# Optimization experiments

Hardware: AMD Instinct MI355X
Metric: run time of the kernel (lower is better)

## Reference

```python
import jax, jax.numpy as jnp
import numpy as np

NUM_HEADS = 32
HEAD_DIM = 128
NUM_KV_HEADS = 8
SCALE = 0.08838834764831845  # 1/sqrt(128)
SEQ_LEN = 2048
TOTAL_TOKENS = 4096  # batch=2 sequences of 2048


def setup_inputs() -> dict:
    key = jax.random.key(0)
    kq, kk, kv = jax.random.split(key, 3)
    q = jax.random.normal(kq, (TOTAL_TOKENS, NUM_HEADS * HEAD_DIM), dtype=jnp.float32)
    k = jax.random.normal(kk, (TOTAL_TOKENS, NUM_KV_HEADS * HEAD_DIM), dtype=jnp.float32)
    v = jax.random.normal(kv, (TOTAL_TOKENS, NUM_KV_HEADS * HEAD_DIM), dtype=jnp.float32)
    return {"q": q, "k": k, "v": v, "seq_len": SEQ_LEN}


def reference(q, k, v, seq_len):
    # Unified (varlen) causal GQA attention: flattened tokens are split into
    # batch sequences of equal length (the prefill path of the unified kernel).
    T = q.shape[0]
    B = T // seq_len
    G = NUM_HEADS // NUM_KV_HEADS  # query heads per kv head
    # [B, S, Hkv, G, D] and [B, S, Hkv, D]
    qh = q.reshape(B, seq_len, NUM_KV_HEADS, G, HEAD_DIM)
    kh = k.reshape(B, seq_len, NUM_KV_HEADS, HEAD_DIM)
    vh = v.reshape(B, seq_len, NUM_KV_HEADS, HEAD_DIM)
    # scores: [B, Hkv, G, Sq, Sk]
    scores = jnp.einsum("bqhgd,bkhd->bhgqk", qh, kh) * SCALE
    causal = jnp.tril(jnp.ones((seq_len, seq_len), dtype=bool))
    scores = jnp.where(causal, scores, jnp.finfo(scores.dtype).min)
    probs = jax.nn.softmax(scores, axis=-1)
    # out: [B, Sq, Hkv, G, D]
    o = jnp.einsum("bhgqk,bkhd->bqhgd", probs, vh)
    return o.reshape(T, NUM_HEADS * HEAD_DIM)
```

## Files before the change

kernel.cpp:

```cpp
#include <hip/hip_runtime.h>
#include <stdint.h>
#include <stddef.h>


#define S_LEN   2048
#define HQ      32
#define HKV     8
#define DH      128
#define QSTRIDE (HQ*DH)
#define KSTRIDE (HKV*DH)
#define SCALE_L2 0.12751139830213113f

#define KTILE      64
#define NTILES     (S_LEN/KTILE)
#define CSTRIDE    520
#define KPART      (16*CSTRIDE)
#define TILE_ELEMS (KPART + 16*CSTRIDE)

typedef __bf16 bf16;
typedef short        s16x4 __attribute__((ext_vector_type(4)));
typedef short        s16x8 __attribute__((ext_vector_type(8)));
typedef float        f32x4 __attribute__((ext_vector_type(4)));
typedef unsigned int u32x4 __attribute__((ext_vector_type(4)));

__device__ __forceinline__ unsigned int pk2(float a, float b) {
  union { bf16 h[2]; unsigned int u; } x;
  x.h[0] = (bf16)a; x.h[1] = (bf16)b;
  return x.u;
}

__device__ __forceinline__ int koff(int chunk, int key) {
  return chunk*CSTRIDE + key*8;
}
__device__ __forceinline__ int voff(int unit, int d) {
  return KPART + unit*CSTRIDE + d*4;
}

__global__ __launch_bounds__(512, 4)
void attn_fwd(const float* __restrict__ qg, const float* __restrict__ kg,
              const float* __restrict__ vg, float* __restrict__ og) {
  __shared__ bf16 smem[2*TILE_ELEMS];

  const int tid   = threadIdx.x;
  const int lane  = tid & 63;
  const int wave  = tid >> 6;
  const int l15   = lane & 15;
  const int quad  = lane >> 4;
  const int pairp = blockIdx.x;
  const int h     = blockIdx.y;
  const int b     = blockIdx.z;
  const int hkv   = h >> 2;

  const int fk_key = tid >> 3, fk_cg = tid & 7;
  const int fv_u   = tid & 15, fv_dq = tid >> 4;
  float4 fkx[4], fvx[4];

  auto load_regs = [&](int t) {
    const float* kp = kg + (size_t)(b*S_LEN + t*KTILE + fk_key)*KSTRIDE
                         + hkv*DH + fk_cg*16;
#pragma unroll
    for (int i = 0; i < 4; ++i) fkx[i] = ((const float4*)kp)[i];
    const int d0 = fv_dq*4;
#pragma unroll
    for (int j = 0; j < 4; ++j)
      fvx[j] = *(const float4*)(vg + (size_t)(b*S_LEN + t*KTILE + fv_u*4 + j)*KSTRIDE
                                   + hkv*DH + d0);
  };
  auto store_tile = [&](int bi) {
    bf16* kb = smem + bi*TILE_ELEMS;
#pragma unroll
    for (int ii = 0; ii < 2; ++ii) {
      u32x4 w;
      w[0] = pk2(fkx[2*ii].x,   fkx[2*ii].y);   w[1] = pk2(fkx[2*ii].z,   fkx[2*ii].w);
      w[2] = pk2(fkx[2*ii+1].x, fkx[2*ii+1].y); w[3] = pk2(fkx[2*ii+1].z, fkx[2*ii+1].w);
      *(u32x4*)(kb + koff(fk_cg*2 + ii, fk_key)) = w;
    }
    const float* g0 = (const float*)&fvx[0];
    const float* g1 = (const float*)&fvx[1];
    const float* g2 = (const float*)&fvx[2];
    const float* g3 = (const float*)&fvx[3];
#pragma unroll
    for (int i = 0; i < 4; i += 2) {
      u32x4 w;
      w[0] = pk2(g0[i],   g1[i]);
      w[1] = pk2(g2[i],   g3[i]);
      w[2] = pk2(g0[i+1], g1[i+1]);
      w[3] = pk2(g2[i+1], g3[i+1]);
      *(u32x4*)(kb + voff(fv_u, fv_dq*4 + i)) = w;
    }
  };

  f32x4 oacc[9];
  u32x4 qf[4];
  const s16x4 ones = { (short)0x3F80, (short)0x3F80,
                       (short)0x3F80, (short)0x3F80 };

  const int qbs[2] = { pairp, 15 - pairp };
  load_regs(0);

  int gs = 0;
#pragma unroll 1
  for (int item = 0; item < 2; ++item) {
    const int qblk = qbs[item];
    const int qw   = qblk*128 + wave*16;
    const int nst  = qblk*2 + 2;

    {
      const float* qp = qg + (size_t)(b*S_LEN + qw + l15)*QSTRIDE
                           + h*DH + quad*8;
#pragma unroll
      for (int c = 0; c < 4; ++c) {
        const float4 a4 = ((const float4*)(qp + c*32))[0];
        const float4 b4 = ((const float4*)(qp + c*32))[1];
        u32x4 w;
        w[0] = pk2(a4.x*SCALE_L2, a4.y*SCALE_L2);
        w[1] = pk2(a4.z*SCALE_L2, a4.w*SCALE_L2);
        w[2] = pk2(b4.x*SCALE_L2, b4.y*SCALE_L2);
        w[3] = pk2(b4.z*SCALE_L2, b4.w*SCALE_L2);
        qf[c] = w;
      }
    }
#pragma unroll
    for (int nd = 0; nd < 9; ++nd) oacc[nd] = (f32x4){0.f, 0.f, 0.f, 0.f};

#pragma unroll 1
    for (int i = 0; i < nst; ++i, ++gs) {
      const int k0  = i*KTILE;
      const int buf = gs & 1;
      store_tile(buf);
      const bool more  = (i + 1 < nst);
      const bool cross = (!more) && (item == 0);
      if (more)       load_regs(i + 1);
      else if (cross) load_regs(0);
      __syncthreads();

      if (k0 <= qw + 15) {
        const bf16* kb = smem + buf*TILE_ELEMS;

        f32x4 sacc[4];
#pragma unroll
        for (int mt = 0; mt < 4; ++mt) sacc[mt] = (f32x4){0.f, 0.f, 0.f, 0.f};
#pragma unroll
        for (int c = 0; c < 4; ++c) {
#pragma unroll
          for (int mt = 0; mt < 4; ++mt) {
            const u32x4 af = *(const u32x4*)(kb + koff(c*4 + quad, mt*16 + l15));
            sacc[mt] = __builtin_amdgcn_mfma_f32_16x16x32_bf16(
                __builtin_bit_cast(s16x8, af), __builtin_bit_cast(s16x8, qf[c]),
                sacc[mt], 0, 0, 0);
          }
        }

        if (k0 + KTILE - 1 > qw) {
          const int qgl = qw + l15;
#pragma unroll
          for (int mt = 0; mt < 4; ++mt)
#pragma unroll
            for (int r = 0; r < 4; ++r) {
              const int key = k0 + mt*16 + quad*4 + r;
              if (key > qgl) sacc[mt][r] = -3e38f;
            }
        }
        s16x4 pa[4];
#pragma unroll
        for (int mt = 0; mt < 4; ++mt) {
          union { bf16 hh[4]; s16x4 s; } u;
#pragma unroll
          for (int r = 0; r < 4; ++r)
            u.hh[r] = (bf16)__builtin_amdgcn_exp2f(sacc[mt][r]);
          pa[mt] = u.s;
        }

#pragma unroll
        for (int kt = 0; kt < 4; ++kt) {
#pragma unroll
          for (int nd = 0; nd < 8; ++nd) {
            const s16x4 bv = *(const s16x4*)(kb + voff(kt*4 + quad, nd*16 + l15));
            oacc[nd] = __builtin_amdgcn_mfma_f32_16x16x16bf16_1k(
                pa[kt], bv, oacc[nd], 0, 0, 0);
          }
          oacc[8] = __builtin_amdgcn_mfma_f32_16x16x16bf16_1k(
              pa[kt], ones, oacc[8], 0, 0, 0);
        }
      }
    }

#pragma unroll
    for (int r = 0; r < 4; ++r) {
      const float inv = 1.0f / oacc[8][r];
      const size_t base = (size_t)(b*S_LEN + qw + quad*4 + r)*QSTRIDE
                        + h*DH + l15;
#pragma unroll
      for (int nd = 0; nd < 8; ++nd)
        og[base + nd*16] = oacc[nd][r] * inv;
    }
  }
}

extern "C" void kernel_launch(void* const* d_in, const int* in_sizes, int n_in,
                              void* d_out, int out_size, void* d_ws, size_t ws_size,
                              hipStream_t stream) {
  const float* q = (const float*)d_in[0];
  const float* k = (const float*)d_in[1];
  const float* v = (const float*)d_in[2];
  float* out = (float*)d_out;
  (void)d_ws; (void)ws_size;
  dim3 grid(8, HQ, 2);
  dim3 block(512);
  attn_fwd<<<grid, block, 0, stream>>>(q, k, v, out);
}
```

Before: 251.3 us.

## Prefetch K/V two tiles ahead, store after compute, and widen V LDS reads

Restructures the tile pipeline so the next tile is written to the alternate LDS buffer and the one after is loaded into registers before computing the current tile, with a single barrier at the end of each step. A prologue stages tile 0 and prefetches tile 1, and the cross-item prefetch is folded into a global step counter (TSTEPS). The V layout in LDS is reorganized so each lane reads 8 bf16 values with one 128-bit load, split into two MFMA operands, halving LDS read instructions for V. The exp-to-bf16 packing is also done pairwise. It adds register pressure from holding the prefetched tile and depends on the fixed total step count being correct.

```diff
diff --git a/kernel.cpp b/kernel.cpp
--- a/kernel.cpp
+++ b/kernel.cpp
@@ -16,11 +16,13 @@
 #define CSTRIDE    520
 #define KPART      (16*CSTRIDE)
 #define TILE_ELEMS (KPART + 16*CSTRIDE)
+#define TSTEPS     34
 
 typedef __bf16 bf16;
 typedef short        s16x4 __attribute__((ext_vector_type(4)));
 typedef short        s16x8 __attribute__((ext_vector_type(8)));
 typedef float        f32x4 __attribute__((ext_vector_type(4)));
+typedef unsigned int u32x2 __attribute__((ext_vector_type(2)));
 typedef unsigned int u32x4 __attribute__((ext_vector_type(4)));
 
 __device__ __forceinline__ unsigned int pk2(float a, float b) {
@@ -31,9 +33,6 @@
 
 __device__ __forceinline__ int koff(int chunk, int key) {
   return chunk*CSTRIDE + key*8;
-}
-__device__ __forceinline__ int voff(int unit, int d) {
-  return KPART + unit*CSTRIDE + d*4;
 }
 
 __global__ __launch_bounds__(512, 4)
@@ -75,18 +74,19 @@
       w[2] = pk2(fkx[2*ii+1].x, fkx[2*ii+1].y); w[3] = pk2(fkx[2*ii+1].z, fkx[2*ii+1].w);
       *(u32x4*)(kb + koff(fk_cg*2 + ii, fk_key)) = w;
     }
+    bf16* vb = kb + KPART;
     const float* g0 = (const float*)&fvx[0];
     const float* g1 = (const float*)&fvx[1];
     const float* g2 = (const float*)&fvx[2];
     const float* g3 = (const float*)&fvx[3];
 #pragma unroll
-    for (int i = 0; i < 4; i += 2) {
-      u32x4 w;
-      w[0] = pk2(g0[i],   g1[i]);
-      w[1] = pk2(g2[i],   g3[i]);
-      w[2] = pk2(g0[i+1], g1[i+1]);
-      w[3] = pk2(g2[i+1], g3[i+1]);
-      *(u32x4*)(kb + voff(fv_u, fv_dq*4 + i)) = w;
+    for (int i = 0; i < 4; ++i) {
+      const int d = fv_dq*4 + i;
+      u32x2 w;
+      w[0] = pk2(g0[i], g1[i]);
+      w[1] = pk2(g2[i], g3[i]);
+      *(u32x2*)(vb + fv_u*CSTRIDE + (d >> 5)*128 + (d & 15)*8
+                   + ((d >> 4) & 1)*4) = w;
     }
   };
 
@@ -96,7 +96,12 @@
                        (short)0x3F80, (short)0x3F80 };
 
   const int qbs[2] = { pairp, 15 - pairp };
+  const int nst0   = qbs[0]*2 + 2;
+
   load_regs(0);
+  store_tile(0);
+  load_regs(1);
+  __syncthreads();
 
   int gs = 0;
 #pragma unroll 1
@@ -127,15 +132,13 @@
     for (int i = 0; i < nst; ++i, ++gs) {
       const int k0  = i*KTILE;
       const int buf = gs & 1;
-      store_tile(buf);
-      const bool more  = (i + 1 < nst);
-      const bool cross = (!more) && (item == 0);
-      if (more)       load_regs(i + 1);
-      else if (cross) load_regs(0);
-      __syncthreads();
+      const int g1 = gs + 1, g2 = gs + 2;
+      if (g1 < TSTEPS) store_tile(buf ^ 1);
+      if (g2 < TSTEPS) load_regs(g2 < nst0 ? g2 : g2 - nst0);
 
       if (k0 <= qw + 15) {
         const bf16* kb = smem + buf*TILE_ELEMS;
+        const bf16* vb = kb + KPART;
 
         f32x4 sacc[4];
 #pragma unroll
@@ -164,25 +167,32 @@
         s16x4 pa[4];
 #pragma unroll
         for (int mt = 0; mt < 4; ++mt) {
-          union { bf16 hh[4]; s16x4 s; } u;
-#pragma unroll
-          for (int r = 0; r < 4; ++r)
-            u.hh[r] = (bf16)__builtin_amdgcn_exp2f(sacc[mt][r]);
+          union { unsigned int uu[2]; s16x4 s; } u;
+          u.uu[0] = pk2(__builtin_amdgcn_exp2f(sacc[mt][0]),
+                        __builtin_amdgcn_exp2f(sacc[mt][1]));
+          u.uu[1] = pk2(__builtin_amdgcn_exp2f(sacc[mt][2]),
+                        __builtin_amdgcn_exp2f(sacc[mt][3]));
           pa[mt] = u.s;
         }
 
 #pragma unroll
         for (int kt = 0; kt < 4; ++kt) {
-#pragma unroll
-          for (int nd = 0; nd < 8; ++nd) {
-            const s16x4 bv = *(const s16x4*)(kb + voff(kt*4 + quad, nd*16 + l15));
-            oacc[nd] = __builtin_amdgcn_mfma_f32_16x16x16bf16_1k(
-                pa[kt], bv, oacc[nd], 0, 0, 0);
+          const bf16* vu = vb + (kt*4 + quad)*CSTRIDE + l15*8;
+#pragma unroll
+          for (int m = 0; m < 4; ++m) {
+            const s16x8 v8 = *(const s16x8*)(vu + m*128);
+            const s16x4 blo = __builtin_shufflevector(v8, v8, 0, 1, 2, 3);
+            const s16x4 bhi = __builtin_shufflevector(v8, v8, 4, 5, 6, 7);
+            oacc[2*m]   = __builtin_amdgcn_mfma_f32_16x16x16bf16_1k(
+                pa[kt], blo, oacc[2*m],   0, 0, 0);
+            oacc[2*m+1] = __builtin_amdgcn_mfma_f32_16x16x16bf16_1k(
+                pa[kt], bhi, oacc[2*m+1], 0, 0, 0);
           }
           oacc[8] = __builtin_amdgcn_mfma_f32_16x16x16bf16_1k(
               pa[kt], ones, oacc[8], 0, 0, 0);
         }
       }
+      __syncthreads();
     }
 
 #pragma unroll
```

After: 250.5 us. Within noise of the previous version (-0.3%).
